# Kernel tuning notes

Measured on AMD Instinct MI355X. Metric: run time of the kernel, lower is better.

Reference implementation:

```python
import jax, jax.numpy as jnp
import numpy as np

LOC = 200 * 200 + 1   # location vocab
E = 100               # loc_emb_size
H = 100               # hidden_neurons (== input size of STLSTM)
D = 12                # temporal/spatial slot embedding dim
NSLOT = 92


def setup_inputs() -> dict:
    key = jax.random.key(0)
    ks = jax.random.split(key, 24)
    B, T = 1024, 256
    inp = {}
    inp["traj"] = jax.random.randint(ks[0], (B, T), 0, LOC)
    inp["lennew"] = jax.random.randint(ks[1], (B, T), 0, T)
    inp["traj_len"] = 255  # static scalar (loop runs traj_len+1 steps)
    inp["tu"] = jax.random.randint(ks[2], (B, T), 0, NSLOT)
    inp["tl"] = jax.random.randint(ks[3], (B, T), 0, NSLOT)
    inp["tu_slot"] = jax.random.randint(ks[4], (B, T), 0, NSLOT)
    inp["tl_slot"] = jax.random.randint(ks[5], (B, T), 0, NSLOT)
    inp["su"] = jax.random.randint(ks[6], (B, T), 0, NSLOT)
    inp["sl"] = jax.random.randint(ks[7], (B, T), 0, NSLOT)
    inp["su_slot"] = jax.random.randint(ks[8], (B, T), 0, NSLOT)
    inp["sl_slot"] = jax.random.randint(ks[9], (B, T), 0, NSLOT)
    # learned parameters
    inp["emb_loc"] = jax.random.normal(ks[10], (LOC, E), jnp.float32) * 0.02
    inp["emb_t"] = jax.random.normal(ks[11], (NSLOT, D), jnp.float32) * 0.02
    inp["emb_s"] = jax.random.normal(ks[12], (NSLOT, D), jnp.float32) * 0.02
    inp["W_ih"] = jax.random.normal(ks[13], (E, 4 * H), jnp.float32) * 0.05
    inp["W_hh"] = jax.random.normal(ks[14], (H, 4 * H), jnp.float32) * 0.05
    inp["b"] = jnp.zeros((4 * H,), jnp.float32)
    inp["W_xt"] = jax.random.normal(ks[15], (E, H), jnp.float32) * 0.05
    inp["W_tt"] = jax.random.normal(ks[16], (D, H), jnp.float32) * 0.05
    inp["b_t"] = jnp.zeros((H,), jnp.float32)
    inp["W_xs"] = jax.random.normal(ks[17], (E, H), jnp.float32) * 0.05
    inp["W_ss"] = jax.random.normal(ks[18], (D, H), jnp.float32) * 0.05
    inp["b_s"] = jnp.zeros((H,), jnp.float32)
    return inp


def reference(traj, lennew, traj_len, tu, tl, tu_slot, tl_slot, su, sl,
              su_slot, sl_slot, emb_loc, emb_t, emb_s, W_ih, W_hh, b,
              W_xt, W_tt, b_t, W_xs, W_ss, b_s):
    steps = int(traj_len) + 1  # static python int -> static slice
    x = emb_loc[traj[:, :steps]]            # [B, S, E] (dropout is identity in eval)
    dtype = x.dtype

    def interp(up_e, low_e, up_d, low_d):
        # linear interpolation between upper/lower slot embeddings
        up = up_d[:, :steps].astype(dtype)[..., None]
        low = low_d[:, :steps].astype(dtype)[..., None]
        return (up * low_e + low * up_e) / jnp.maximum(up + low, 1.0)

    Tq = interp(emb_t[tu[:, :steps]], emb_t[tl[:, :steps]], tu_slot, tl_slot)  # [B,S,D]
    Sq = interp(emb_s[su[:, :steps]], emb_s[sl[:, :steps]], su_slot, sl_slot)  # [B,S,D]

    B = traj.shape[0]
    h0 = jnp.zeros((B, H), dtype)
    c0 = jnp.zeros((B, H), dtype)
    xs = (x.swapaxes(0, 1), Tq.swapaxes(0, 1), Sq.swapaxes(0, 1))  # time-major

    def step(carry, inp):
        h, c = carry
        xt, tg, sg = inp
        gates = xt @ W_ih + h @ W_hh + b           # [B, 4H]
        i, f, g, o = jnp.split(gates, 4, axis=-1)
        i = jax.nn.sigmoid(i)
        f = jax.nn.sigmoid(f)
        g = jnp.tanh(g)
        o = jax.nn.sigmoid(o)
        tgate = jax.nn.sigmoid(xt @ W_xt + tg @ W_tt + b_t)  # temporal gate
        sgate = jax.nn.sigmoid(xt @ W_xs + sg @ W_ss + b_s)  # spatial gate
        c = f * c + i * tgate * sgate * g
        h = o * jnp.tanh(c)
        return (h, c), None

    (h, c), _ = jax.lax.scan(step, (h0, c0), xs)
    # model returns h at index traj_len, which is the final hidden state
    return h
```

## Files before the change

### kernel.cpp

```cpp
#include <hip/hip_runtime.h>

#define B_    1024
#define T_    256
#define LOCN  40001
#define E_    100
#define H_    100
#define NC    600

typedef float f32x2 __attribute__((ext_vector_type(2)));

__device__ __forceinline__ float fsig(float x) {
    const float e = __builtin_amdgcn_exp2f(x * -1.442695040888963f);
    return __builtin_amdgcn_rcpf(1.f + e);
}

constexpr int PROWS = 16;
constexpr int PPAD  = 20;
constexpr int PB    = 256;

__global__ __launch_bounds__(PB) void proj_loc_kernel(
    const float* __restrict__ emb_loc,
    const float* __restrict__ W_ih,
    const float* __restrict__ W_xt,
    const float* __restrict__ W_xs,
    const float* __restrict__ b,
    const float* __restrict__ b_t,
    const float* __restrict__ b_s,
    float* __restrict__ P)
{
    __shared__ __attribute__((aligned(16))) float aT[E_][PPAD];
    const int tid  = threadIdx.x;
    const int row0 = blockIdx.x * PROWS;

    for (int i = tid; i < PROWS * E_; i += PB) {
        const int r = i / E_, k = i - r * E_;
        const int rr = row0 + r;
        aT[k][r] = (rr < LOCN) ? emb_loc[rr * E_ + k] : 0.f;
    }
    __syncthreads();
    if (tid >= 150) return;

    const int c = tid * 4;
    const float* wp; int stride; const float* bp;
    if (c < 400)      { wp = W_ih + c;         stride = 400; bp = b   + c;       }
    else if (c < 500) { wp = W_xt + (c - 400); stride = 100; bp = b_t + c - 400; }
    else              { wp = W_xs + (c - 500); stride = 100; bp = b_s + c - 500; }

    const float4 bias = *(const float4*)bp;
    f32x2 a01[PROWS], a23[PROWS];
    #pragma unroll
    for (int r = 0; r < PROWS; ++r) {
        a01[r] = (f32x2){bias.x, bias.y};
        a23[r] = (f32x2){bias.z, bias.w};
    }

    #pragma unroll 2
    for (int k = 0; k < E_; ++k) {
        const float4 wv = *(const float4*)(wp + (size_t)k * stride);
        const f32x2 w01 = {wv.x, wv.y};
        const f32x2 w23 = {wv.z, wv.w};
        #pragma unroll
        for (int r4 = 0; r4 < PROWS / 4; ++r4) {
            const float4 hv = *(const float4*)(&aT[k][r4 * 4]);
            const f32x2 h0 = {hv.x, hv.x};
            const f32x2 h1 = {hv.y, hv.y};
            const f32x2 h2 = {hv.z, hv.z};
            const f32x2 h3 = {hv.w, hv.w};
            a01[r4 * 4 + 0] = h0 * w01 + a01[r4 * 4 + 0];
            a23[r4 * 4 + 0] = h0 * w23 + a23[r4 * 4 + 0];
            a01[r4 * 4 + 1] = h1 * w01 + a01[r4 * 4 + 1];
            a23[r4 * 4 + 1] = h1 * w23 + a23[r4 * 4 + 1];
            a01[r4 * 4 + 2] = h2 * w01 + a01[r4 * 4 + 2];
            a23[r4 * 4 + 2] = h2 * w23 + a23[r4 * 4 + 2];
            a01[r4 * 4 + 3] = h3 * w01 + a01[r4 * 4 + 3];
            a23[r4 * 4 + 3] = h3 * w23 + a23[r4 * 4 + 3];
        }
    }

    #pragma unroll
    for (int r = 0; r < PROWS; ++r) {
        const int rr = row0 + r;
        if (rr < LOCN) {
            float4 o;
            o.x = a01[r].x; o.y = a01[r].y; o.z = a23[r].x; o.w = a23[r].y;
            *(float4*)(&P[(size_t)rr * NC + c]) = o;
        }
    }
}

__global__ void proj_ts_kernel(
    const float* __restrict__ emb_t, const float* __restrict__ emb_s,
    const float* __restrict__ W_tt,  const float* __restrict__ W_ss,
    float* __restrict__ P_t, float* __restrict__ P_s)
{
    int idx = blockIdx.x * 256 + threadIdx.x;
    if (idx >= 2 * 92 * H_) return;
    int which = idx / (92 * H_);
    int rem   = idx - which * (92 * H_);
    int r = rem / H_, c = rem - r * H_;
    const float* e = which ? emb_s : emb_t;
    const float* W = which ? W_ss : W_tt;
    float acc = 0.f;
    #pragma unroll
    for (int k = 0; k < 12; ++k) acc += e[r * 12 + k] * W[k * H_ + c];
    (which ? P_s : P_t)[rem] = acc;
}

constexpr int RB = 4;
constexpr int NT = 704;

__global__ __launch_bounds__(NT, 3) void lstm_rec_kernel(
    const int* __restrict__ traj,
    const int* __restrict__ traj_len_p,
    const int* __restrict__ tu,      const int* __restrict__ tl,
    const int* __restrict__ tu_slot, const int* __restrict__ tl_slot,
    const int* __restrict__ su,      const int* __restrict__ sl,
    const int* __restrict__ su_slot, const int* __restrict__ sl_slot,
    const float* __restrict__ P,
    const float* __restrict__ P_t,
    const float* __restrict__ P_s,
    const float* __restrict__ W_hh,
    float* __restrict__ out)
{
    __shared__ __attribute__((aligned(16))) float h_lds[RB][H_];
    __shared__ float gates_lds[RB][400];
    __shared__ float tg_lds[RB][H_];
    __shared__ float sg_lds[RB][H_];
    __shared__ int   loc_lds[2][RB];

    const int tid = threadIdx.x;
    const int b0  = blockIdx.x * RB;
    int steps = traj_len_p[0] + 1;
    if (steps > T_) steps = T_;

    f32x2 w2[50];
    if (tid < 400) {
        #pragma unroll
        for (int j = 0; j < 50; ++j) {
            w2[j].x = W_hh[(2 * j)     * 400 + tid];
            w2[j].y = W_hh[(2 * j + 1) * 400 + tid];
        }
        ((float*)h_lds)[tid] = 0.f;
    }
    if (tid < RB) loc_lds[0][tid] = traj[(b0 + tid) * T_];

    const int er = tid / 100;
    const int eh = tid - er * 100;
    float c_reg = 0.f, hval = 0.f;
    __syncthreads();

    for (int t = 0; t < steps; ++t) {
        const int buf = t & 1;

        if (tid >= 700) {
            int r = tid - 700;
            if (t + 1 < steps) loc_lds[buf ^ 1][r] = traj[(b0 + r) * T_ + t + 1];
        }

        if (tid < 400) {
            const int n = tid;
            float gacc[RB];
            #pragma unroll
            for (int r = 0; r < RB; ++r) {
                const int loc = __builtin_amdgcn_readfirstlane(loc_lds[buf][r]);
                const float* __restrict__ Prow = P + (size_t)loc * NC;
                gacc[r] = Prow[n];
            }

            f32x2 acc2[RB];
            #pragma unroll
            for (int r = 0; r < RB; ++r) acc2[r] = (f32x2){0.f, 0.f};
            #pragma unroll
            for (int k4 = 0; k4 < H_ / 4; ++k4) {
                #pragma unroll
                for (int r = 0; r < RB; ++r) {
                    const float4 hv = *(const float4*)(&h_lds[r][k4 * 4]);
                    const f32x2 hlo = {hv.x, hv.y};
                    const f32x2 hhi = {hv.z, hv.w};
                    acc2[r] = hlo * w2[2 * k4]     + acc2[r];
                    acc2[r] = hhi * w2[2 * k4 + 1] + acc2[r];
                }
            }
            const bool isg = (n >= 200 && n < 300);
            #pragma unroll
            for (int r = 0; r < RB; ++r) {
                float v  = (acc2[r].x + acc2[r].y) + gacc[r];
                float xx = isg ? 2.f * v : v;
                float s  = fsig(xx);
                gates_lds[r][n] = isg ? (2.f * s - 1.f) : s;
            }
        }

        if (tid >= 448 && tid < 648) {
            const int  ch   = tid - 448;
            const bool is_t = ch < 100;
            const int  hx   = is_t ? ch : ch - 100;
            const int* up_a = is_t ? tu_slot : su_slot;
            const int* lo_a = is_t ? tl_slot : sl_slot;
            const int* ui_a = is_t ? tu : su;
            const int* li_a = is_t ? tl : sl;
            const float* Pq = is_t ? P_t : P_s;
            float* dst      = is_t ? &tg_lds[0][0] : &sg_lds[0][0];
            #pragma unroll
            for (int r = 0; r < RB; ++r) {
                const int off = __builtin_amdgcn_readfirstlane((b0 + r) * T_ + t);
                const int loc = __builtin_amdgcn_readfirstlane(loc_lds[buf][r]);
                const float* __restrict__ Prow = P + (size_t)loc * NC;
                float gp  = Prow[400 + ch];
                float up  = (float)up_a[off];
                float low = (float)lo_a[off];
                int   ui  = ui_a[off], li = li_a[off];
                const float inv = __builtin_amdgcn_rcpf(fmaxf(up + low, 1.f));
                float iv  = (up * Pq[li * H_ + hx] + low * Pq[ui * H_ + hx]) * inv;
                float pre = gp + iv;
                dst[r * H_ + hx] = fsig(pre);
            }
        }
        __syncthreads();

        if (tid < 400) {
            float i_g = gates_lds[er][eh];
            float f_g = gates_lds[er][100 + eh];
            float g_g = gates_lds[er][200 + eh];
            float o_g = gates_lds[er][300 + eh];
            float tsg = tg_lds[er][eh] * sg_lds[er][eh];
            c_reg = f_g * c_reg + i_g * tsg * g_g;
            hval  = o_g * (2.f * fsig(2.f * c_reg) - 1.f);
            h_lds[er][eh] = hval;
        }
        __syncthreads();
    }

    if (tid < 400) out[b0 * H_ + tid] = hval;
}

extern "C" void kernel_launch(void* const* d_in, const int* in_sizes, int n_in,
                              void* d_out, int out_size, void* d_ws, size_t ws_size,
                              hipStream_t stream) {
    const int*   traj     = (const int*)  d_in[0];
    const int*   traj_len = (const int*)  d_in[2];
    const int*   tu       = (const int*)  d_in[3];
    const int*   tl       = (const int*)  d_in[4];
    const int*   tu_slot  = (const int*)  d_in[5];
    const int*   tl_slot  = (const int*)  d_in[6];
    const int*   su       = (const int*)  d_in[7];
    const int*   sl       = (const int*)  d_in[8];
    const int*   su_slot  = (const int*)  d_in[9];
    const int*   sl_slot  = (const int*)  d_in[10];
    const float* emb_loc  = (const float*)d_in[11];
    const float* emb_t    = (const float*)d_in[12];
    const float* emb_s    = (const float*)d_in[13];
    const float* W_ih     = (const float*)d_in[14];
    const float* W_hh     = (const float*)d_in[15];
    const float* b        = (const float*)d_in[16];
    const float* W_xt     = (const float*)d_in[17];
    const float* W_tt     = (const float*)d_in[18];
    const float* b_t      = (const float*)d_in[19];
    const float* W_xs     = (const float*)d_in[20];
    const float* W_ss     = (const float*)d_in[21];
    const float* b_s      = (const float*)d_in[22];

    float* P   = (float*)d_ws;
    float* P_t = P + (size_t)LOCN * NC;
    float* P_s = P_t + 92 * H_;

    proj_loc_kernel<<<(LOCN + PROWS - 1) / PROWS, PB, 0, stream>>>(
        emb_loc, W_ih, W_xt, W_xs, b, b_t, b_s, P);
    proj_ts_kernel<<<(2 * 92 * H_ + 255) / 256, 256, 0, stream>>>(
        emb_t, emb_s, W_tt, W_ss, P_t, P_s);
    lstm_rec_kernel<<<B_ / RB, NT, 0, stream>>>(
        traj, traj_len, tu, tl, tu_slot, tl_slot, su, sl, su_slot, sl_slot,
        P, P_t, P_s, W_hh, (float*)d_out);
}
```

Before: 722.1 us.

## Fold slot projection into location projection kernel and retile thread work

Removes the separate proj_ts kernel launch by assigning the small time/space slot projection to one extra block of the location projection kernel. The projection GEMM's thread mapping changes so each thread computes 8 rows by 8 columns instead of 16 rows by 4 columns. Each weight load now serves two column groups, and each shared-memory read of the embedding covers fewer rows. The aim is to save one launch and to change the register and load balance in the projection, which precomputes a 40001x600 table. That table is large and its writes likely dominate, so the effect may be small.

```diff
diff --git a/kernel.cpp b/kernel.cpp
--- a/kernel.cpp
+++ b/kernel.cpp
@@ -17,6 +17,7 @@
 constexpr int PROWS = 16;
 constexpr int PPAD  = 20;
 constexpr int PB    = 256;
+constexpr int NBLK  = (LOCN + PROWS - 1) / PROWS;
 
 __global__ __launch_bounds__(PB) void proj_loc_kernel(
     const float* __restrict__ emb_loc,
@@ -26,8 +27,29 @@
     const float* __restrict__ b,
     const float* __restrict__ b_t,
     const float* __restrict__ b_s,
-    float* __restrict__ P)
+    const float* __restrict__ emb_t,
+    const float* __restrict__ emb_s,
+    const float* __restrict__ W_tt,
+    const float* __restrict__ W_ss,
+    float* __restrict__ P,
+    float* __restrict__ P_t,
+    float* __restrict__ P_s)
 {
+    if (blockIdx.x == NBLK) {
+        for (int idx = threadIdx.x; idx < 2 * 92 * H_; idx += PB) {
+            const int which = idx / (92 * H_);
+            const int rem   = idx - which * (92 * H_);
+            const int r = rem / H_, c = rem - r * H_;
+            const float* e = which ? emb_s : emb_t;
+            const float* W = which ? W_ss : W_tt;
+            float acc = 0.f;
+            #pragma unroll
+            for (int k = 0; k < 12; ++k) acc += e[r * 12 + k] * W[k * H_ + c];
+            (which ? P_s : P_t)[rem] = acc;
+        }
+        return;
+    }
+
     __shared__ __attribute__((aligned(16))) float aT[E_][PPAD];
     const int tid  = threadIdx.x;
     const int row0 = blockIdx.x * PROWS;
@@ -40,70 +62,63 @@
     __syncthreads();
     if (tid >= 150) return;
 
-    const int c = tid * 4;
-    const float* wp; int stride; const float* bp;
-    if (c < 400)      { wp = W_ih + c;         stride = 400; bp = b   + c;       }
-    else if (c < 500) { wp = W_xt + (c - 400); stride = 100; bp = b_t + c - 400; }
-    else              { wp = W_xs + (c - 500); stride = 100; bp = b_s + c - 500; }
-
-    const float4 bias = *(const float4*)bp;
-    f32x2 a01[PROWS], a23[PROWS];
+    const int rh = tid & 1;
+    const int cg = tid >> 1;
+    const int c  = cg * 8;
+    const int r0 = rh * 8;
+
+    const float *wpA, *wpB, *bpA, *bpB; int strA, strB;
+    {
+        const int cA = c, cB = c + 4;
+        if (cA < 400)      { wpA = W_ih + cA;         strA = 400; bpA = b   + cA;       }
+        else if (cA < 500) { wpA = W_xt + (cA - 400); strA = 100; bpA = b_t + cA - 400; }
+        else               { wpA = W_xs + (cA - 500); strA = 100; bpA = b_s + cA - 500; }
+        if (cB < 400)      { wpB = W_ih + cB;         strB = 400; bpB = b   + cB;       }
+        else if (cB < 500) { wpB = W_xt + (cB - 400); strB = 100; bpB = b_t + cB - 400; }
+        else               { wpB = W_xs + (cB - 500); strB = 100; bpB = b_s + cB - 500; }
+    }
+
+    const float4 bA = *(const float4*)bpA;
+    const float4 bB = *(const float4*)bpB;
+    f32x2 aAl[8], aAh[8], aBl[8], aBh[8];
     #pragma unroll
-    for (int r = 0; r < PROWS; ++r) {
-        a01[r] = (f32x2){bias.x, bias.y};
-        a23[r] = (f32x2){bias.z, bias.w};
+    for (int r = 0; r < 8; ++r) {
+        aAl[r] = (f32x2){bA.x, bA.y};
+        aAh[r] = (f32x2){bA.z, bA.w};
+        aBl[r] = (f32x2){bB.x, bB.y};
+        aBh[r] = (f32x2){bB.z, bB.w};
     }
 
     #pragma unroll 2
     for (int k = 0; k < E_; ++k) {
-        const float4 wv = *(const float4*)(wp + (size_t)k * stride);
-        const f32x2 w01 = {wv.x, wv.y};
-        const f32x2 w23 = {wv.z, wv.w};
+        const float4 wA = *(const float4*)(wpA + (size_t)k * strA);
+        const float4 wB = *(const float4*)(wpB + (size_t)k * strB);
+        const f32x2 wA01 = {wA.x, wA.y}, wA23 = {wA.z, wA.w};
+        const f32x2 wB01 = {wB.x, wB.y}, wB23 = {wB.z, wB.w};
+        const float4 h0 = *(const float4*)(&aT[k][r0]);
+        const float4 h1 = *(const float4*)(&aT[k][r0 + 4]);
+        const float hs[8] = {h0.x, h0.y, h0.z, h0.w, h1.x, h1.y, h1.z, h1.w};
         #pragma unroll
-        for (int r4 = 0; r4 < PROWS / 4; ++r4) {
-            const float4 hv = *(const float4*)(&aT[k][r4 * 4]);
-            const f32x2 h0 = {hv.x, hv.x};
-            const f32x2 h1 = {hv.y, hv.y};
-            const f32x2 h2 = {hv.z, hv.z};
-            const f32x2 h3 = {hv.w, hv.w};
-            a01[r4 * 4 + 0] = h0 * w01 + a01[r4 * 4 + 0];
-            a23[r4 * 4 + 0] = h0 * w23 + a23[r4 * 4 + 0];
-            a01[r4 * 4 + 1] = h1 * w01 + a01[r4 * 4 + 1];
-            a23[r4 * 4 + 1] = h1 * w23 + a23[r4 * 4 + 1];
-            a01[r4 * 4 + 2] = h2 * w01 + a01[r4 * 4 + 2];
-            a23[r4 * 4 + 2] = h2 * w23 + a23[r4 * 4 + 2];
-            a01[r4 * 4 + 3] = h3 * w01 + a01[r4 * 4 + 3];
-            a23[r4 * 4 + 3] = h3 * w23 + a23[r4 * 4 + 3];
+        for (int r = 0; r < 8; ++r) {
+            const f32x2 hh = {hs[r], hs[r]};
+            aAl[r] = hh * wA01 + aAl[r];
+            aAh[r] = hh * wA23 + aAh[r];
+            aBl[r] = hh * wB01 + aBl[r];
+            aBh[r] = hh * wB23 + aBh[r];
         }
     }
 
     #pragma unroll
-    for (int r = 0; r < PROWS; ++r) {
-        const int rr = row0 + r;
+    for (int r = 0; r < 8; ++r) {
+        const int rr = row0 + r0 + r;
         if (rr < LOCN) {
-            float4 o;
-            o.x = a01[r].x; o.y = a01[r].y; o.z = a23[r].x; o.w = a23[r].y;
-            *(float4*)(&P[(size_t)rr * NC + c]) = o;
-        }
-    }
-}
-
-__global__ void proj_ts_kernel(
-    const float* __restrict__ emb_t, const float* __restrict__ emb_s,
-    const float* __restrict__ W_tt,  const float* __restrict__ W_ss,
-    float* __restrict__ P_t, float* __restrict__ P_s)
-{
-    int idx = blockIdx.x * 256 + threadIdx.x;
-    if (idx >= 2 * 92 * H_) return;
-    int which = idx / (92 * H_);
-    int rem   = idx - which * (92 * H_);
-    int r = rem / H_, c = rem - r * H_;
-    const float* e = which ? emb_s : emb_t;
-    const float* W = which ? W_ss : W_tt;
-    float acc = 0.f;
-    #pragma unroll
-    for (int k = 0; k < 12; ++k) acc += e[r * 12 + k] * W[k * H_ + c];
-    (which ? P_s : P_t)[rem] = acc;
+            float4 o1, o2;
+            o1.x = aAl[r].x; o1.y = aAl[r].y; o1.z = aAh[r].x; o1.w = aAh[r].y;
+            o2.x = aBl[r].x; o2.y = aBl[r].y; o2.z = aBh[r].x; o2.w = aBh[r].y;
+            *(float4*)(&P[(size_t)rr * NC + c])     = o1;
+            *(float4*)(&P[(size_t)rr * NC + c + 4]) = o2;
+        }
+    }
 }
 
 constexpr int RB = 4;
@@ -264,10 +279,9 @@
     float* P_t = P + (size_t)LOCN * NC;
     float* P_s = P_t + 92 * H_;
 
-    proj_loc_kernel<<<(LOCN + PROWS - 1) / PROWS, PB, 0, stream>>>(
-        emb_loc, W_ih, W_xt, W_xs, b, b_t, b_s, P);
-    proj_ts_kernel<<<(2 * 92 * H_ + 255) / 256, 256, 0, stream>>>(
-        emb_t, emb_s, W_tt, W_ss, P_t, P_s);
+    proj_loc_kernel<<<NBLK + 1, PB, 0, stream>>>(
+        emb_loc, W_ih, W_xt, W_xs, b, b_t, b_s,
+        emb_t, emb_s, W_tt, W_ss, P, P_t, P_s);
     lstm_rec_kernel<<<B_ / RB, NT, 0, stream>>>(
         traj, traj_len, tu, tl, tu_slot, tl_slot, su, sl, su_slot, sl_slot,
         P, P_t, P_s, W_hh, (float*)d_out);
```

New measurement: 773.4 us. 7.1% more time.
